# Kernel optimization log

Hardware: AMD Instinct MI355X
Metric: run time of the kernel (lower is better)

The kernel has to match this reference:

```python
import jax, jax.numpy as jnp
import numpy as np

N_NODES = 100000
N_EDGES = 3200000
IN_EDGE = 2      # input_edge_features_size
IN_NODE = 2      # input_node_features_size
H0 = 10          # hidden_edge_features_sizes[0]
H1 = 10          # hidden_edge_features_sizes[1]
OUT = 2          # output_size of fully_connected_nodes


def _linear_params(key, fan_in, fan_out):
    # torch.nn.Linear default init: U(-1/sqrt(fan_in), 1/sqrt(fan_in))
    k1, k2 = jax.random.split(key)
    bound = 1.0 / np.sqrt(fan_in)
    W = jax.random.uniform(k1, (fan_in, fan_out), minval=-bound, maxval=bound, dtype=jnp.float32)
    b = jax.random.uniform(k2, (fan_out,), minval=-bound, maxval=bound, dtype=jnp.float32)
    return W, b


def setup_inputs() -> dict:
    key = jax.random.key(0)
    ks = jax.random.split(key, 6)
    node_features = jax.random.normal(ks[0], (N_NODES, IN_NODE), dtype=jnp.float32)
    edge_features = jax.random.normal(ks[1], (N_EDGES, IN_EDGE), dtype=jnp.float32)
    edge_index = jax.random.randint(ks[2], (2, N_EDGES), 0, N_NODES, dtype=jnp.int64)
    # fully_connected_edges: Linear(2 -> 10)
    We, be = _linear_params(ks[3], IN_EDGE, H0)
    # DTSP_EdgeUpdate: edge MLP over [edge_feat(10) | src_node(2) | dst_node(2)] -> 10
    Wu, bu = _linear_params(ks[4], H0 + 2 * IN_NODE, H1)
    # fully_connected_nodes: Linear(2 -> 2)
    Wn, bn = _linear_params(ks[5], IN_NODE, OUT)
    return {"node_features": node_features, "edge_features": edge_features,
            "edge_index": edge_index, "We": We, "be": be, "Wu": Wu, "bu": bu,
            "Wn": Wn, "bn": bn}


def reference(node_features, edge_features, edge_index, We, be, Wu, bu, Wn, bn):
    row, col = edge_index[0], edge_index[1]
    # edge_features = self.fully_connected_edges(edge_features)  # [E, 10]
    ef = edge_features @ We + be
    # DTSP_EdgeUpdate: gather endpoint node features per edge, concat, Linear -> [E, 10]
    src = node_features[row]                       # [E, 2] gather
    dst = node_features[col]                       # [E, 2] gather
    ef = jnp.concatenate([ef, src, dst], axis=-1) @ Wu + bu  # [E, 10]
    # Original forward returns only the node branch (edge branch is unused):
    out = node_features @ Wn + bn                  # [N, 2]
    # return both so the gather+MLP edge path is not dead code under jit
    return out, ef
```

## Files before the change

kernel.cpp:

```cpp
#include <hip/hip_runtime.h>

#define N_NODES 100000
#define N_EDGES 3200000

typedef float f4_t __attribute__((ext_vector_type(4)));

__global__ __launch_bounds__(256) void gnn_fused_kernel(
    const float* __restrict__ node, const float* __restrict__ edge,
    const int* __restrict__ ei,
    const float* __restrict__ We, const float* __restrict__ be,
    const float* __restrict__ Wu, const float* __restrict__ bu,
    const float* __restrict__ Wn, const float* __restrict__ bn,
    float* __restrict__ out, float* __restrict__ ef_out)
{
    __shared__ float wf[4][80];
    __shared__ float stg[4][64 * 21];

    const int tid   = threadIdx.x;
    const int lane  = tid & 63;
    const int wslot = tid >> 6;
    const int T     = blockIdx.x * 256 + tid;
    const int gwave = blockIdx.x * 4 + wslot;
    const size_t E0 = (size_t)gwave * 256;

    const bool is64 = (ei[1] == 0) & (ei[3] == 0) & (ei[5] == 0) & (ei[7] == 0);

    float4 eA = ((const float4*)edge)[E0 / 2 + lane];
    float4 eB = ((const float4*)edge)[E0 / 2 + 64 + lane];

    int r0, r1, r2, r3, c0, c1, c2, c3;
    if (is64) {
        const int4* R = (const int4*)ei;
        const int4* C = (const int4*)(ei + 2 * (size_t)N_EDGES);
        int4 ra = R[E0 / 2 + lane], rb = R[E0 / 2 + 64 + lane];
        int4 ca = C[E0 / 2 + lane], cb = C[E0 / 2 + 64 + lane];
        r0 = ra.x; r1 = ra.z; r2 = rb.x; r3 = rb.z;
        c0 = ca.x; c1 = ca.z; c2 = cb.x; c3 = cb.z;
    } else {
        const int2* R = (const int2*)ei;
        const int2* C = (const int2*)(ei + (size_t)N_EDGES);
        int2 ra = R[E0 / 2 + lane], rb = R[E0 / 2 + 64 + lane];
        int2 ca = C[E0 / 2 + lane], cb = C[E0 / 2 + 64 + lane];
        r0 = ra.x; r1 = ra.y; r2 = rb.x; r3 = rb.y;
        c0 = ca.x; c1 = ca.y; c2 = cb.x; c3 = cb.y;
    }

    if (T < N_NODES) {
        float2 nf = ((const float2*)node)[T];
        float o0 = fmaf(nf.y, Wn[2], fmaf(nf.x, Wn[0], bn[0]));
        float o1 = fmaf(nf.y, Wn[3], fmaf(nf.x, Wn[1], bn[1]));
        ((float2*)out)[T] = make_float2(o0, o1);
    }

    if (lane < 60) {
        int r = lane / 10, h = lane % 10;
        float v;
        if (r < 2) {
            v = 0.0f;
            #pragma unroll
            for (int k = 0; k < 10; ++k) v = fmaf(We[r * 10 + k], Wu[k * 10 + h], v);
        } else {
            v = Wu[(10 + (r - 2)) * 10 + h];
        }
        wf[wslot][8 * h + r] = v;
    }
    if (lane < 10) {
        int h = lane;
        float v = bu[h];
        #pragma unroll
        for (int k = 0; k < 10; ++k) v = fmaf(be[k], Wu[k * 10 + h], v);
        wf[wslot][8 * h + 6] = v;
    }
    __builtin_amdgcn_wave_barrier();

    float2 s0 = ((const float2*)node)[r0];
    float2 d0 = ((const float2*)node)[c0];
    float2 s1 = ((const float2*)node)[r1];
    float2 d1 = ((const float2*)node)[c1];
    float2 s2 = ((const float2*)node)[r2];
    float2 d2 = ((const float2*)node)[c2];
    float2 s3 = ((const float2*)node)[r3];
    float2 d3 = ((const float2*)node)[c3];

    float* S = &stg[wslot][0];
    const float* WF = &wf[wslot][0];
    f4_t* g4 = (f4_t*)ef_out + (size_t)gwave * 640;

    {
        float rr[20];
        #pragma unroll
        for (int h = 0; h < 10; ++h) {
            const f4_t* wv = (const f4_t*)&WF[8 * h];
            f4_t wa = wv[0];
            f4_t wb = wv[1];
            float a0 = wb.z, a1 = wb.z;
            a0 = fmaf(eA.x, wa.x, a0);  a1 = fmaf(eA.z, wa.x, a1);
            a0 = fmaf(eA.y, wa.y, a0);  a1 = fmaf(eA.w, wa.y, a1);
            a0 = fmaf(s0.x, wa.z, a0);  a1 = fmaf(s1.x, wa.z, a1);
            a0 = fmaf(s0.y, wa.w, a0);  a1 = fmaf(s1.y, wa.w, a1);
            a0 = fmaf(d0.x, wb.x, a0);  a1 = fmaf(d1.x, wb.x, a1);
            a0 = fmaf(d0.y, wb.y, a0);  a1 = fmaf(d1.y, wb.y, a1);
            rr[h] = a0; rr[10 + h] = a1;
        }
        #pragma unroll
        for (int k = 0; k < 20; ++k) S[lane * 21 + k] = rr[k];
        __builtin_amdgcn_wave_barrier();
        #pragma unroll
        for (int v = 0; v < 5; ++v) {
            unsigned slot = v * 64 + lane;
            unsigned p = slot / 5u, jj = slot - 5u * p;
            const float* src = &S[p * 21 + 4 * jj];
            f4_t w = { src[0], src[1], src[2], src[3] };
            __builtin_nontemporal_store(w, &g4[slot]);
        }
        __builtin_amdgcn_wave_barrier();
    }
    {
        float rr[20];
        #pragma unroll
        for (int h = 0; h < 10; ++h) {
            const f4_t* wv = (const f4_t*)&WF[8 * h];
            f4_t wa = wv[0];
            f4_t wb = wv[1];
            float a0 = wb.z, a1 = wb.z;
            a0 = fmaf(eB.x, wa.x, a0);  a1 = fmaf(eB.z, wa.x, a1);
            a0 = fmaf(eB.y, wa.y, a0);  a1 = fmaf(eB.w, wa.y, a1);
            a0 = fmaf(s2.x, wa.z, a0);  a1 = fmaf(s3.x, wa.z, a1);
            a0 = fmaf(s2.y, wa.w, a0);  a1 = fmaf(s3.y, wa.w, a1);
            a0 = fmaf(d2.x, wb.x, a0);  a1 = fmaf(d3.x, wb.x, a1);
            a0 = fmaf(d2.y, wb.y, a0);  a1 = fmaf(d3.y, wb.y, a1);
            rr[h] = a0; rr[10 + h] = a1;
        }
        #pragma unroll
        for (int k = 0; k < 20; ++k) S[lane * 21 + k] = rr[k];
        __builtin_amdgcn_wave_barrier();
        #pragma unroll
        for (int v = 0; v < 5; ++v) {
            unsigned slot = v * 64 + lane;
            unsigned p = slot / 5u, jj = slot - 5u * p;
            const float* src = &S[p * 21 + 4 * jj];
            f4_t w = { src[0], src[1], src[2], src[3] };
            __builtin_nontemporal_store(w, &g4[320 + slot]);
        }
    }
}

extern "C" void kernel_launch(void* const* d_in, const int* in_sizes, int n_in,
                              void* d_out, int out_size, void* d_ws, size_t ws_size,
                              hipStream_t stream) {
    const float* node = (const float*)d_in[0];
    const float* edge = (const float*)d_in[1];
    const int*   ei   = (const int*)d_in[2];
    const float* We   = (const float*)d_in[3];
    const float* be   = (const float*)d_in[4];
    const float* Wu   = (const float*)d_in[5];
    const float* bu   = (const float*)d_in[6];
    const float* Wn   = (const float*)d_in[7];
    const float* bn   = (const float*)d_in[8];

    float* out = (float*)d_out;
    float* ef  = out + 2 * (size_t)N_NODES;

    hipLaunchKernelGGL(gnn_fused_kernel, dim3(N_EDGES / 1024), dim3(256), 0, stream,
                       node, edge, ei, We, be, Wu, bu, Wn, bn, out, ef);
}
```

Before: 43.25 us.

## Map one edge per lane across four chunks and hoist all gathers

Each lane now handles one edge in each of four 64-edge chunks instead of two adjacent edges per lane. This shrinks the LDS staging buffer and lets all eight node gathers be issued up front, before the weight-fold setup, to overlap latency. The edge-index and edge-feature loads become narrower, scalar and float2, and the output stores switch from nontemporal to regular stores. That may change cache behaviour on the large streaming write and adds more load instructions.

```diff
diff --git a/kernel.cpp b/kernel.cpp
--- a/kernel.cpp
+++ b/kernel.cpp
@@ -14,7 +14,7 @@
     float* __restrict__ out, float* __restrict__ ef_out)
 {
     __shared__ float wf[4][80];
-    __shared__ float stg[4][64 * 21];
+    __shared__ float stg[4][64 * 11];
 
     const int tid   = threadIdx.x;
     const int lane  = tid & 63;
@@ -25,24 +25,33 @@
 
     const bool is64 = (ei[1] == 0) & (ei[3] == 0) & (ei[5] == 0) & (ei[7] == 0);
 
-    float4 eA = ((const float4*)edge)[E0 / 2 + lane];
-    float4 eB = ((const float4*)edge)[E0 / 2 + 64 + lane];
+    float2 ef[4];
+    #pragma unroll
+    for (int k = 0; k < 4; ++k)
+        ef[k] = ((const float2*)edge)[E0 + 64 * k + lane];
 
-    int r0, r1, r2, r3, c0, c1, c2, c3;
+    int rI[4], cI[4];
     if (is64) {
-        const int4* R = (const int4*)ei;
-        const int4* C = (const int4*)(ei + 2 * (size_t)N_EDGES);
-        int4 ra = R[E0 / 2 + lane], rb = R[E0 / 2 + 64 + lane];
-        int4 ca = C[E0 / 2 + lane], cb = C[E0 / 2 + 64 + lane];
-        r0 = ra.x; r1 = ra.z; r2 = rb.x; r3 = rb.z;
-        c0 = ca.x; c1 = ca.z; c2 = cb.x; c3 = cb.z;
+        #pragma unroll
+        for (int k = 0; k < 4; ++k) {
+            size_t e = E0 + 64 * k + lane;
+            rI[k] = ei[2 * e];
+            cI[k] = ei[2 * ((size_t)N_EDGES + e)];
+        }
     } else {
-        const int2* R = (const int2*)ei;
-        const int2* C = (const int2*)(ei + (size_t)N_EDGES);
-        int2 ra = R[E0 / 2 + lane], rb = R[E0 / 2 + 64 + lane];
-        int2 ca = C[E0 / 2 + lane], cb = C[E0 / 2 + 64 + lane];
-        r0 = ra.x; r1 = ra.y; r2 = rb.x; r3 = rb.y;
-        c0 = ca.x; c1 = ca.y; c2 = cb.x; c3 = cb.y;
+        #pragma unroll
+        for (int k = 0; k < 4; ++k) {
+            size_t e = E0 + 64 * k + lane;
+            rI[k] = ei[e];
+            cI[k] = ei[(size_t)N_EDGES + e];
+        }
+    }
+
+    float2 sv[4], dv[4];
+    #pragma unroll
+    for (int k = 0; k < 4; ++k) {
+        sv[k] = ((const float2*)node)[rI[k]];
+        dv[k] = ((const float2*)node)[cI[k]];
     }
 
     if (T < N_NODES) {
@@ -73,75 +82,50 @@
     }
     __builtin_amdgcn_wave_barrier();
 
-    float2 s0 = ((const float2*)node)[r0];
-    float2 d0 = ((const float2*)node)[c0];
-    float2 s1 = ((const float2*)node)[r1];
-    float2 d1 = ((const float2*)node)[c1];
-    float2 s2 = ((const float2*)node)[r2];
-    float2 d2 = ((const float2*)node)[c2];
-    float2 s3 = ((const float2*)node)[r3];
-    float2 d3 = ((const float2*)node)[c3];
-
     float* S = &stg[wslot][0];
     const float* WF = &wf[wslot][0];
-    f4_t* g4 = (f4_t*)ef_out + (size_t)gwave * 640;
 
-    {
-        float rr[20];
+    #pragma unroll
+    for (int k = 0; k < 4; ++k) {
+        float o[10];
         #pragma unroll
         for (int h = 0; h < 10; ++h) {
             const f4_t* wv = (const f4_t*)&WF[8 * h];
             f4_t wa = wv[0];
             f4_t wb = wv[1];
-            float a0 = wb.z, a1 = wb.z;
-            a0 = fmaf(eA.x, wa.x, a0);  a1 = fmaf(eA.z, wa.x, a1);
-            a0 = fmaf(eA.y, wa.y, a0);  a1 = fmaf(eA.w, wa.y, a1);
-            a0 = fmaf(s0.x, wa.z, a0);  a1 = fmaf(s1.x, wa.z, a1);
-            a0 = fmaf(s0.y, wa.w, a0);  a1 = fmaf(s1.y, wa.w, a1);
-            a0 = fmaf(d0.x, wb.x, a0);  a1 = fmaf(d1.x, wb.x, a1);
-            a0 = fmaf(d0.y, wb.y, a0);  a1 = fmaf(d1.y, wb.y, a1);
-            rr[h] = a0; rr[10 + h] = a1;
+            float a = wb.z;
+            a = fmaf(ef[k].x, wa.x, a);
+            a = fmaf(ef[k].y, wa.y, a);
+            a = fmaf(sv[k].x, wa.z, a);
+            a = fmaf(sv[k].y, wa.w, a);
+            a = fmaf(dv[k].x, wb.x, a);
+            a = fmaf(dv[k].y, wb.y, a);
+            o[h] = a;
         }
         #pragma unroll
-        for (int k = 0; k < 20; ++k) S[lane * 21 + k] = rr[k];
+        for (int m = 0; m < 10; ++m) S[lane * 11 + m] = o[m];
         __builtin_amdgcn_wave_barrier();
-        #pragma unroll
-        for (int v = 0; v < 5; ++v) {
-            unsigned slot = v * 64 + lane;
-            unsigned p = slot / 5u, jj = slot - 5u * p;
-            const float* src = &S[p * 21 + 4 * jj];
-            f4_t w = { src[0], src[1], src[2], src[3] };
-            __builtin_nontemporal_store(w, &g4[slot]);
+
+        f4_t* g4 = (f4_t*)ef_out + (size_t)gwave * 640 + k * 160;
+        {
+            unsigned f = 4u * lane;
+            f4_t w = { S[f + f / 10u], S[(f+1) + (f+1) / 10u],
+                       S[(f+2) + (f+2) / 10u], S[(f+3) + (f+3) / 10u] };
+            g4[lane] = w;
+        }
+        {
+            unsigned f = 4u * (lane + 64);
+            f4_t w = { S[f + f / 10u], S[(f+1) + (f+1) / 10u],
+                       S[(f+2) + (f+2) / 10u], S[(f+3) + (f+3) / 10u] };
+            g4[lane + 64] = w;
+        }
+        if (lane < 32) {
+            unsigned f = 4u * (lane + 128);
+            f4_t w = { S[f + f / 10u], S[(f+1) + (f+1) / 10u],
+                       S[(f+2) + (f+2) / 10u], S[(f+3) + (f+3) / 10u] };
+            g4[lane + 128] = w;
         }
         __builtin_amdgcn_wave_barrier();
-    }
-    {
-        float rr[20];
-        #pragma unroll
-        for (int h = 0; h < 10; ++h) {
-            const f4_t* wv = (const f4_t*)&WF[8 * h];
-            f4_t wa = wv[0];
-            f4_t wb = wv[1];
-            float a0 = wb.z, a1 = wb.z;
-            a0 = fmaf(eB.x, wa.x, a0);  a1 = fmaf(eB.z, wa.x, a1);
-            a0 = fmaf(eB.y, wa.y, a0);  a1 = fmaf(eB.w, wa.y, a1);
-            a0 = fmaf(s2.x, wa.z, a0);  a1 = fmaf(s3.x, wa.z, a1);
-            a0 = fmaf(s2.y, wa.w, a0);  a1 = fmaf(s3.y, wa.w, a1);
-            a0 = fmaf(d2.x, wb.x, a0);  a1 = fmaf(d3.x, wb.x, a1);
-            a0 = fmaf(d2.y, wb.y, a0);  a1 = fmaf(d3.y, wb.y, a1);
-            rr[h] = a0; rr[10 + h] = a1;
-        }
-        #pragma unroll
-        for (int k = 0; k < 20; ++k) S[lane * 21 + k] = rr[k];
-        __builtin_amdgcn_wave_barrier();
-        #pragma unroll
-        for (int v = 0; v < 5; ++v) {
-            unsigned slot = v * 64 + lane;
-            unsigned p = slot / 5u, jj = slot - 5u * p;
-            const float* src = &S[p * 21 + 4 * jj];
-            f4_t w = { src[0], src[1], src[2], src[3] };
-            __builtin_nontemporal_store(w, &g4[320 + slot]);
-        }
     }
 }
 
@@ -159,8 +143,8 @@
     const float* bn   = (const float*)d_in[8];
 
     float* out = (float*)d_out;
-    float* ef  = out + 2 * (size_t)N_NODES;
+    float* efo = out + 2 * (size_t)N_NODES;
 
     hipLaunchKernelGGL(gnn_fused_kernel, dim3(N_EDGES / 1024), dim3(256), 0, stream,
-                       node, edge, ei, We, be, Wu, bu, Wn, bn, out, ef);
+                       node, edge, ei, We, be, Wu, bu, Wn, bn, out, efo);
 }
```

After: 46.39 us. 7.3% more time.
